# Kernel optimization log

Hardware: AMD Instinct MI355X
Metric: run time of the kernel (lower is better)

The kernel has to match this reference:

```python
import jax, jax.numpy as jnp
import numpy as np

N = 16384

def setup_inputs() -> dict:
    key = jax.random.key(0)
    k1, k2, k3 = jax.random.split(key, 3)
    risk = jax.random.normal(k1, (N,), dtype=jnp.float32)
    time = jax.random.uniform(k2, (N,), dtype=jnp.float32)
    event = jax.random.randint(k3, (N,), 0, 2).astype(jnp.float32)
    return {"risk": risk, "time": time, "event": event}

def reference(risk, time, event):
    theta = risk.reshape(-1)  # [n]
    # Risk-set mask: R[i, j] = 1.0 iff time[j] >= time[i]  (same as the torch double loop)
    R_mat = (time[None, :] >= time[:, None]).astype(theta.dtype)  # [n, n]
    exp_theta = jnp.exp(theta)  # [n]
    log_risk_set = jnp.log(R_mat @ exp_theta)  # [n]
    loss = -((theta - log_risk_set) * event).sum() / event.sum()
    return loss
```

## Files before the change

kernel.cpp:

```cpp
#include <hip/hip_runtime.h>

#define NR    16
#define LOCB  1024
#define CAP   1536
#define BLK   1024

__device__ __forceinline__ int keyof(float t) {
    int k = (int)(t * 16384.f);
    return k < 0 ? 0 : (k > 16383 ? 16383 : k);
}

__global__ __launch_bounds__(BLK)
void cox_bin(const float* __restrict__ risk,
             const float* __restrict__ tm,
             const float* __restrict__ event,
             float4* __restrict__ staged,
             int* __restrict__ cnt16,
             float* __restrict__ sum16,
             float* __restrict__ evs16,
             int n) {
    __shared__ int   lc[NR];
    __shared__ float lsum[NR];
    __shared__ int   lofs[NR];
    __shared__ float sev[BLK / 64];
    const int tid  = threadIdx.x;
    const int lane = tid & 63;
    const int wave = tid >> 6;

    if (tid < NR) { lc[tid] = 0; lsum[tid] = 0.f; }
    __syncthreads();

    const int j = blockIdx.x * BLK + tid;
    const bool act = (j < n);
    float t = 0.f, rk = 0.f, ev = 0.f, e = 0.f;
    int r = 0, lpos = 0;
    if (act) {
        t  = tm[j];
        rk = risk[j];
        ev = event[j];
        e  = __expf(rk);
        r  = keyof(t) >> 10;
        lpos = atomicAdd(&lc[r], 1);
        atomicAdd(&lsum[r], e);
    }
    float evv = act ? ev : 0.f;
    #pragma unroll
    for (int o = 32; o > 0; o >>= 1) evv += __shfl_down(evv, o);
    if (lane == 0) sev[wave] = evv;
    __syncthreads();

    if (tid == 0) {
        int o = 0;
        #pragma unroll
        for (int q = 0; q < NR; ++q) { lofs[q] = o; o += lc[q]; }
        float s = 0.f;
        #pragma unroll
        for (int w = 0; w < BLK / 64; ++w) s += sev[w];
        evs16[blockIdx.x] = s;
    }
    if (tid < NR) {
        cnt16[blockIdx.x * NR + tid] = lc[tid];
        sum16[blockIdx.x * NR + tid] = lsum[tid];
    }
    __syncthreads();
    if (act)
        staged[blockIdx.x * BLK + lofs[r] + lpos] = make_float4(t, e, rk, ev);
}

__global__ __launch_bounds__(BLK)
void cox_solve(const float4* __restrict__ staged,
               const int* __restrict__ cnt16,
               const float* __restrict__ sum16,
               const float* __restrict__ evs16,
               float* __restrict__ out) {
    __shared__ int    cnt[LOCB];
    __shared__ int    off[LOCB];
    __shared__ float  bsm[LOCB];
    __shared__ float2 TE[CAP];
    __shared__ int    segbase[NR], seglen[NR], P[NR + 1];
    __shared__ float  wsc[16], wsc2[16], sn[16], sd[16];
    __shared__ float  s_gsuf, s_den;
    const int g    = blockIdx.x;
    const int tid  = threadIdx.x;
    const int lane = tid & 63;
    const int wave = tid >> 6;

    cnt[tid] = 0; bsm[tid] = 0.f;
    if (tid == 0) { s_gsuf = 0.f; s_den = 0.f; }
    __syncthreads();

    if (tid < NR) {
        int base = 0;
        for (int r = 0; r < g; ++r) base += cnt16[tid * NR + r];
        segbase[tid] = base;
        seglen[tid]  = cnt16[tid * NR + g];
        atomicAdd(&s_den, evs16[tid]);
    }
    if (tid < NR * NR) {
        const int b = tid >> 4, r = tid & (NR - 1);
        if (r > g) atomicAdd(&s_gsuf, sum16[b * NR + r]);
    }
    __syncthreads();
    if (tid == 0) {
        int p = 0;
        #pragma unroll
        for (int b = 0; b < NR; ++b) { P[b] = p; p += seglen[b]; }
        P[NR] = p;
    }
    __syncthreads();
    const int m = P[NR];
    const float gsuf = s_gsuf;

    float4 el[2]; int lb[2]; int nel = 0;
    for (int idx = tid; idx < m; idx += BLK) {
        int b = 0;
        while (P[b + 1] <= idx) ++b;
        const float4 v = staged[b * BLK + segbase[b] + (idx - P[b])];
        el[nel] = v;
        const int lbk = keyof(v.x) & (LOCB - 1);
        lb[nel] = lbk;
        atomicAdd(&cnt[lbk], 1);
        atomicAdd(&bsm[lbk], v.y);
        ++nel;
    }
    __syncthreads();

    {
        const int   c = cnt[tid];
        const float e = bsm[tid];
        int incl = c;
        #pragma unroll
        for (int o = 1; o < 64; o <<= 1) {
            const int tmp = __shfl_up(incl, o);
            if (lane >= o) incl += tmp;
        }
        float fincl = e;
        #pragma unroll
        for (int o = 1; o < 64; o <<= 1) {
            const float tmp = __shfl_down(fincl, o);
            if (lane + o < 64) fincl += tmp;
        }
        if (lane == 63) wsc[wave]  = (float)incl;
        if (lane == 0)  wsc2[wave] = fincl;
        __syncthreads();
        int croff = 0;
        for (int w = 0; w < wave; ++w) croff += (int)wsc[w];
        float crsuf = 0.f;
        for (int w = wave + 1; w < 16; ++w) crsuf += wsc2[w];
        off[tid] = croff + incl - c;
        bsm[tid] = crsuf + (fincl - e);
    }
    __syncthreads();

    for (int k = 0; k < nel; ++k) {
        const int pos = atomicAdd(&off[lb[k]], 1);
        TE[pos] = make_float2(el[k].x, el[k].y);
    }
    __syncthreads();

    float num = 0.f;
    for (int k = 0; k < nel; ++k) {
        const int b     = lb[k];
        const int end   = off[b];
        const int start = end - cnt[b];
        const float t   = el[k].x;
        float corr = 0.f;
        for (int q = start; q < end; ++q) {
            const float2 te = TE[q];
            corr += (te.x >= t) ? te.y : 0.f;
        }
        num += (el[k].z - logf(gsuf + bsm[b] + corr)) * el[k].w;
    }

    #pragma unroll
    for (int o = 32; o > 0; o >>= 1) num += __shfl_down(num, o);
    if (lane == 0) sn[wave] = num;
    __syncthreads();
    if (tid == 0) {
        float tn = 0.f;
        #pragma unroll
        for (int w = 0; w < 16; ++w) tn += sn[w];
        atomicAdd(out, -tn / s_den);
    }
}

extern "C" void kernel_launch(void* const* d_in, const int* in_sizes, int n_in,
                              void* d_out, int out_size, void* d_ws, size_t ws_size,
                              hipStream_t stream) {
    const float* risk  = (const float*)d_in[0];
    const float* tm    = (const float*)d_in[1];
    const float* event = (const float*)d_in[2];
    float* out = (float*)d_out;
    const int n = in_sizes[0];

    float4* staged = (float4*)d_ws;
    int*    cnt16  = (int*)(staged + NR * BLK);
    float*  sum16  = (float*)(cnt16 + NR * NR);
    float*  evs16  = sum16 + NR * NR;

    const int nb1 = (n + BLK - 1) / BLK;
    cox_bin  <<<nb1, BLK, 0, stream>>>(risk, tm, event, staged, cnt16, sum16, evs16, n);
    cox_solve<<<NR,  BLK, 0, stream>>>(staged, cnt16, sum16, evs16, out);
}
```

Measured before the change: 69.65 us.

## Fuse binning and solve into one kernel with redundant full-input scan per block

Removes the separate binning kernel and its global staging buffer. Each of the 16 blocks now reads the whole input with float4 loads, computes the event sum and the suffix exp-sum for later time ranges itself, and gathers its own range's elements into shared memory through an atomic counter. This saves a kernel launch and the global round trip, but every block redundantly reads all inputs and does exp work. It also adds contention on a single shared-memory atomic and assumes no range holds more than CAP elements and that n is divisible by 4.

Result: faster. 65.68 us (-5.7%).

```diff
diff --git a/kernel.cpp b/kernel.cpp
--- a/kernel.cpp
+++ b/kernel.cpp
@@ -11,74 +11,17 @@
 }
 
 __global__ __launch_bounds__(BLK)
-void cox_bin(const float* __restrict__ risk,
+void cox_one(const float* __restrict__ risk,
              const float* __restrict__ tm,
              const float* __restrict__ event,
-             float4* __restrict__ staged,
-             int* __restrict__ cnt16,
-             float* __restrict__ sum16,
-             float* __restrict__ evs16,
-             int n) {
-    __shared__ int   lc[NR];
-    __shared__ float lsum[NR];
-    __shared__ int   lofs[NR];
-    __shared__ float sev[BLK / 64];
-    const int tid  = threadIdx.x;
-    const int lane = tid & 63;
-    const int wave = tid >> 6;
-
-    if (tid < NR) { lc[tid] = 0; lsum[tid] = 0.f; }
-    __syncthreads();
-
-    const int j = blockIdx.x * BLK + tid;
-    const bool act = (j < n);
-    float t = 0.f, rk = 0.f, ev = 0.f, e = 0.f;
-    int r = 0, lpos = 0;
-    if (act) {
-        t  = tm[j];
-        rk = risk[j];
-        ev = event[j];
-        e  = __expf(rk);
-        r  = keyof(t) >> 10;
-        lpos = atomicAdd(&lc[r], 1);
-        atomicAdd(&lsum[r], e);
-    }
-    float evv = act ? ev : 0.f;
-    #pragma unroll
-    for (int o = 32; o > 0; o >>= 1) evv += __shfl_down(evv, o);
-    if (lane == 0) sev[wave] = evv;
-    __syncthreads();
-
-    if (tid == 0) {
-        int o = 0;
-        #pragma unroll
-        for (int q = 0; q < NR; ++q) { lofs[q] = o; o += lc[q]; }
-        float s = 0.f;
-        #pragma unroll
-        for (int w = 0; w < BLK / 64; ++w) s += sev[w];
-        evs16[blockIdx.x] = s;
-    }
-    if (tid < NR) {
-        cnt16[blockIdx.x * NR + tid] = lc[tid];
-        sum16[blockIdx.x * NR + tid] = lsum[tid];
-    }
-    __syncthreads();
-    if (act)
-        staged[blockIdx.x * BLK + lofs[r] + lpos] = make_float4(t, e, rk, ev);
-}
-
-__global__ __launch_bounds__(BLK)
-void cox_solve(const float4* __restrict__ staged,
-               const int* __restrict__ cnt16,
-               const float* __restrict__ sum16,
-               const float* __restrict__ evs16,
-               float* __restrict__ out) {
+             float* __restrict__ out, int n) {
+    __shared__ float4 S4[CAP];
     __shared__ int    cnt[LOCB];
     __shared__ int    off[LOCB];
     __shared__ float  bsm[LOCB];
     __shared__ float2 TE[CAP];
-    __shared__ int    segbase[NR], seglen[NR], P[NR + 1];
-    __shared__ float  wsc[16], wsc2[16], sn[16], sd[16];
+    __shared__ float  wsc[16], wsc2[16], sn[16];
+    __shared__ int    s_m;
     __shared__ float  s_gsuf, s_den;
     const int g    = blockIdx.x;
     const int tid  = threadIdx.x;
@@ -86,42 +29,54 @@
     const int wave = tid >> 6;
 
     cnt[tid] = 0; bsm[tid] = 0.f;
-    if (tid == 0) { s_gsuf = 0.f; s_den = 0.f; }
+    if (tid == 0) { s_m = 0; s_gsuf = 0.f; s_den = 0.f; }
     __syncthreads();
 
-    if (tid < NR) {
-        int base = 0;
-        for (int r = 0; r < g; ++r) base += cnt16[tid * NR + r];
-        segbase[tid] = base;
-        seglen[tid]  = cnt16[tid * NR + g];
-        atomicAdd(&s_den, evs16[tid]);
+    const float4* tm4 = (const float4*)tm;
+    const float4* rk4 = (const float4*)risk;
+    const float4* ev4 = (const float4*)event;
+    const int nq = n >> 2;
+    float gsufp = 0.f, denp = 0.f;
+    for (int q = tid; q < nq; q += BLK) {
+        const float4 t4 = tm4[q];
+        const float4 r4 = rk4[q];
+        const float4 e4 = ev4[q];
+        #pragma unroll
+        for (int c = 0; c < 4; ++c) {
+            const float t  = c == 0 ? t4.x : c == 1 ? t4.y : c == 2 ? t4.z : t4.w;
+            const float rk = c == 0 ? r4.x : c == 1 ? r4.y : c == 2 ? r4.z : r4.w;
+            const float ev = c == 0 ? e4.x : c == 1 ? e4.y : c == 2 ? e4.z : e4.w;
+            const int   r  = keyof(t) >> 10;
+            denp += ev;
+            if (r > g) {
+                gsufp += __expf(rk);
+            } else if (r == g) {
+                const float e = __expf(rk);
+                const unsigned long long mask = __ballot(1);
+                (void)mask;
+                const int pos = atomicAdd(&s_m, 1);
+                S4[pos] = make_float4(t, e, rk, ev);
+            }
+        }
     }
-    if (tid < NR * NR) {
-        const int b = tid >> 4, r = tid & (NR - 1);
-        if (r > g) atomicAdd(&s_gsuf, sum16[b * NR + r]);
+    #pragma unroll
+    for (int o = 32; o > 0; o >>= 1) {
+        denp  += __shfl_down(denp, o);
+        gsufp += __shfl_down(gsufp, o);
     }
+    if (lane == 0) { atomicAdd(&s_den, denp); atomicAdd(&s_gsuf, gsufp); }
     __syncthreads();
-    if (tid == 0) {
-        int p = 0;
-        #pragma unroll
-        for (int b = 0; b < NR; ++b) { P[b] = p; p += seglen[b]; }
-        P[NR] = p;
-    }
-    __syncthreads();
-    const int m = P[NR];
+    const int   m    = s_m;
     const float gsuf = s_gsuf;
+    const float den  = s_den;
 
     float4 el[2]; int lb[2]; int nel = 0;
     for (int idx = tid; idx < m; idx += BLK) {
-        int b = 0;
-        while (P[b + 1] <= idx) ++b;
-        const float4 v = staged[b * BLK + segbase[b] + (idx - P[b])];
-        el[nel] = v;
+        const float4 v = S4[idx];
         const int lbk = keyof(v.x) & (LOCB - 1);
-        lb[nel] = lbk;
+        el[nel] = v; lb[nel] = lbk; ++nel;
         atomicAdd(&cnt[lbk], 1);
         atomicAdd(&bsm[lbk], v.y);
-        ++nel;
     }
     __syncthreads();
 
@@ -180,7 +135,7 @@
         float tn = 0.f;
         #pragma unroll
         for (int w = 0; w < 16; ++w) tn += sn[w];
-        atomicAdd(out, -tn / s_den);
+        atomicAdd(out, -tn / den);
     }
 }
 
@@ -193,12 +148,5 @@
     float* out = (float*)d_out;
     const int n = in_sizes[0];
 
-    float4* staged = (float4*)d_ws;
-    int*    cnt16  = (int*)(staged + NR * BLK);
-    float*  sum16  = (float*)(cnt16 + NR * NR);
-    float*  evs16  = sum16 + NR * NR;
-
-    const int nb1 = (n + BLK - 1) / BLK;
-    cox_bin  <<<nb1, BLK, 0, stream>>>(risk, tm, event, staged, cnt16, sum16, evs16, n);
-    cox_solve<<<NR,  BLK, 0, stream>>>(staged, cnt16, sum16, evs16, out);
+    cox_one<<<NR, BLK, 0, stream>>>(risk, tm, event, out, n);
 }
```
